# Optimization experiments

Hardware: AMD Instinct MI355X
Metric: run time of the kernel (lower is better)

## Reference

```python
import jax, jax.numpy as jnp
import numpy as np

OUT = 7  # output_size (RoIPool 7x7)


def _crop_one(fm_all, roi, K):
    """Adaptive max-pool one ROI to [C, OUT, OUT].

    fm_all: [B, C, H, W]; roi: [5] int32 (batch, x1, y1, x2, y2).
    K: static max bin extent (ceil(H/OUT)+1), covers any ROI size.
    Matches torch adaptive_max_pool2d bins: start=floor(i*n/OUT), end=ceil((i+1)*n/OUT).
    """
    H, W = fm_all.shape[2], fm_all.shape[3]
    b, x1, y1, x2, y2 = roi[0], roi[1], roi[2], roi[3], roi[4]
    fm = jnp.take(fm_all, b, axis=0)  # [C, H, W]
    h = y2 - y1
    w = x2 - x1
    o = jnp.arange(OUT)
    ys = y1 + (o * h) // OUT
    ye = y1 + ((o + 1) * h + OUT - 1) // OUT  # ceil div
    xs = x1 + (o * w) // OUT
    xe = x1 + ((o + 1) * w + OUT - 1) // OUT
    k = jnp.arange(K)

    # --- pool along width (separable rectangle max) ---
    col_idx = jnp.clip(xs[:, None] + k[None, :], 0, W - 1)   # [OUT, K]
    col_valid = k[None, :] < (xe - xs)[:, None]              # [OUT, K]
    g = fm[:, :, col_idx]                                    # [C, H, OUT, K]
    g = jnp.where(col_valid, g, -jnp.inf)
    tw = g.max(axis=-1)                                      # [C, H, OUT]

    # --- pool along height ---
    row_idx = jnp.clip(ys[:, None] + k[None, :], 0, H - 1)   # [OUT, K]
    row_valid = k[None, :] < (ye - ys)[:, None]
    g2 = tw[:, row_idx, :]                                   # [C, OUT, K, OUT]
    g2 = jnp.where(row_valid[None, :, :, None], g2, -jnp.inf)
    return g2.max(axis=2)                                    # [C, OUT, OUT]


def setup_inputs() -> dict:
    key = jax.random.key(0)
    B, C, H, W, R = 2, 256, 50, 50, 192
    feature_map = jax.random.normal(key, (B, C, H, W), dtype=jnp.float32)
    rng = np.random.default_rng(0)
    batch = rng.integers(0, B, R)
    x1 = rng.integers(0, W - 1, R)
    x2 = rng.integers(x1 + 1, W + 1)  # ensure x2 > x1, <= W
    y1 = rng.integers(0, H - 1, R)
    y2 = rng.integers(y1 + 1, H + 1)
    rois = jnp.asarray(np.stack([batch, x1, y1, x2, y2], axis=1).astype(np.int32))
    return {"feature_map": feature_map, "rois": rois}


def reference(feature_map, rois):
    H = feature_map.shape[2]
    K = -(-H // OUT) + 1  # static max bin extent
    return jax.vmap(_crop_one, in_axes=(None, 0, None))(feature_map, rois, K)  # [R, C, OUT, OUT]
```

## Files before the change

kernel.cpp:

```cpp
#include <hip/hip_runtime.h>
#include <hip/hip_bf16.h>
#include <math.h>


#define OUT_N 7
#define CPB 4
#define LDS_W 65

__global__ __launch_bounds__(256) void roicrop_kernel(
    const float* __restrict__ fm,
    const int* __restrict__ rois,
    float* __restrict__ out,
    int R, int C, int H, int W)
{
    __shared__ float tw[CPB][OUT_N][LDS_W];

    const int lane = threadIdx.x & 63;
    const int wave = threadIdx.x >> 6;
    const int cg_per_r = C / CPB;
    const int r  = blockIdx.x / cg_per_r;
    const int cg = blockIdx.x % cg_per_r;
    const int c  = cg * CPB + wave;

    const int* roi = rois + r * 5;
    const int b  = roi[0];
    const int x1 = roi[1];
    const int y1 = roi[2];
    const int x2 = roi[3];
    const int y2 = roi[4];
    const int h = y2 - y1;
    const int w = x2 - x1;

    int x = x1 + lane;
    if (lane >= w) x = x1;
    const float* col = fm + (size_t)(b * C + c) * (size_t)(H * W) + x;

    #pragma unroll
    for (int i = 0; i < OUT_N; ++i) {
        const int ys = y1 + (i * h) / OUT_N;
        const int ye = y1 + ((i + 1) * h + OUT_N - 1) / OUT_N;
        float m = -INFINITY;
        const float* p = col + (size_t)ys * W;
        for (int y = ys; y < ye; ++y) {
            m = fmaxf(m, *p);
            p += W;
        }
        tw[wave][i][lane] = m;
    }
    __syncthreads();

    const int t = threadIdx.x;
    if (t < CPB * OUT_N * OUT_N) {
        const int wc = t / (OUT_N * OUT_N);
        const int l  = t % (OUT_N * OUT_N);
        const int i  = l / OUT_N;
        const int j  = l % OUT_N;
        const int xs = (j * w) / OUT_N;
        const int xe = ((j + 1) * w + OUT_N - 1) / OUT_N;
        float m = -INFINITY;
        for (int dx = xs; dx < xe; ++dx) {
            m = fmaxf(m, tw[wc][i][dx]);
        }
        const int cc = cg * CPB + wc;
        out[((size_t)r * C + cc) * (OUT_N * OUT_N) + l] = m;
    }
}

extern "C" void kernel_launch(void* const* d_in, const int* in_sizes, int n_in,
                              void* d_out, int out_size, void* d_ws, size_t ws_size,
                              hipStream_t stream)
{
    const float* fm = (const float*)d_in[0];
    const int* rois = (const int*)d_in[1];
    float* out      = (float*)d_out;

    const int R = in_sizes[1] / 5;
    const int C = out_size / (R * OUT_N * OUT_N);
    const int H = 50;
    const int W = 50;

    const int grid = R * (C / CPB);
    roicrop_kernel<<<grid, 256, 0, stream>>>(fm, rois, out, R, C, H, W);
}
```

Measured before the change: 87.48 us.

## Process two channels per wave with unrolled row loads in RoI pool

Each wave now handles two channels instead of one, so a block covers eight channels and the grid is halved. The vertical max loop is unrolled by two and interleaves loads from both channels, giving more independent memory requests in flight per wave. The output stage loops so 256 threads can cover the 392 outputs. In exchange the block count drops, which may reduce occupancy across the GPU, and register use per thread rises.

```diff
diff --git a/kernel.cpp b/kernel.cpp
--- a/kernel.cpp
+++ b/kernel.cpp
@@ -4,7 +4,7 @@
 
 
 #define OUT_N 7
-#define CPB 4
+#define CPB 8
 #define LDS_W 65
 
 __global__ __launch_bounds__(256) void roicrop_kernel(
@@ -20,7 +20,7 @@
     const int cg_per_r = C / CPB;
     const int r  = blockIdx.x / cg_per_r;
     const int cg = blockIdx.x % cg_per_r;
-    const int c  = cg * CPB + wave;
+    const int c0 = cg * CPB + wave * 2;
 
     const int* roi = rois + r * 5;
     const int b  = roi[0];
@@ -33,26 +33,43 @@
 
     int x = x1 + lane;
     if (lane >= w) x = x1;
-    const float* col = fm + (size_t)(b * C + c) * (size_t)(H * W) + x;
+    const size_t plane = (size_t)(H * W);
+    const float* colA = fm + (size_t)(b * C + c0)     * plane + x;
+    const float* colB = fm + (size_t)(b * C + c0 + 1) * plane + x;
 
     #pragma unroll
     for (int i = 0; i < OUT_N; ++i) {
         const int ys = y1 + (i * h) / OUT_N;
         const int ye = y1 + ((i + 1) * h + OUT_N - 1) / OUT_N;
-        float m = -INFINITY;
-        const float* p = col + (size_t)ys * W;
-        for (int y = ys; y < ye; ++y) {
-            m = fmaxf(m, *p);
-            p += W;
+        const int hb = ye - ys;
+        const float* pa = colA + (size_t)ys * W;
+        const float* pb = colB + (size_t)ys * W;
+        float ma = -INFINITY, mb = -INFINITY;
+        int k = 0;
+        for (; k + 1 < hb; k += 2) {
+            float a0 = pa[0];
+            float a1 = pa[W];
+            float b0 = pb[0];
+            float b1 = pb[W];
+            pa += 2 * W;
+            pb += 2 * W;
+            ma = fmaxf(ma, fmaxf(a0, a1));
+            mb = fmaxf(mb, fmaxf(b0, b1));
         }
-        tw[wave][i][lane] = m;
+        if (k < hb) {
+            ma = fmaxf(ma, pa[0]);
+            mb = fmaxf(mb, pb[0]);
+        }
+        tw[wave * 2 + 0][i][lane] = ma;
+        tw[wave * 2 + 1][i][lane] = mb;
     }
     __syncthreads();
 
     const int t = threadIdx.x;
-    if (t < CPB * OUT_N * OUT_N) {
-        const int wc = t / (OUT_N * OUT_N);
-        const int l  = t % (OUT_N * OUT_N);
+    #pragma unroll
+    for (int o = t; o < CPB * OUT_N * OUT_N; o += 256) {
+        const int wc = o / (OUT_N * OUT_N);
+        const int l  = o % (OUT_N * OUT_N);
         const int i  = l / OUT_N;
         const int j  = l % OUT_N;
         const int xs = (j * w) / OUT_N;
```

Result: faster. 78.24 us (-10.6%).
